# Kernel tuning notes

Hardware: AMD Instinct MI355X
Metric: run time of the kernel (lower is better)

The kernel has to match this reference:

```python
import jax, jax.numpy as jnp
import numpy as np

ALPHA = 3.0   # self.alpha
TAU = 0.1     # contrastive temperature
K = 8         # configs.k (top-k hyperedges per node)


def _scale(x, w, ehy, enod):
    """One scale of incidence_matrix_learn.
    x: [B, L, D] series tokens; w: [ws, D] word tokens;
    ehy: [H, D] hyperedge embedding table; enod: [N, D] node embedding table, N = L + ws.
    Returns (binary incidence matrix [N, H] float32, scalar contrastive loss).
    """
    B = x.shape[0]
    # concat_all[i]: cat(x.permute(0,2,1), word_expanded) -> [B, D, N]
    we = jnp.broadcast_to(w.T[None], (B,) + w.T.shape)          # [B, D, ws]
    concat = jnp.concatenate([jnp.transpose(x, (0, 2, 1)), we], axis=-1)  # [B, D, N]
    N, H = enod.shape[0], ehy.shape[0]
    # adjacency: softmax(relu(alpha * nodeec @ hyperen.T)) along hyperedge dim
    a = enod @ ehy.T                                            # [N, H]
    adj = jax.nn.softmax(jax.nn.relu(ALPHA * a), axis=-1)
    # top-k mask + threshold > 0.5 -> binary incidence matrix
    k = min(H, K)
    _, idx = jax.lax.top_k(adj, k)                              # [N, k]
    mask = jnp.zeros_like(adj).at[jnp.arange(N)[:, None], idx].set(1.0)
    adj_bin = ((adj * mask) > 0.5).astype(jnp.float32)          # [N, H]
    # positives: nodes sharing any hyperedge (build_pos_indices_from_edge_index),
    # equivalent to (A A^T > 0) with self excluded; dropping all-zero columns is a no-op here
    P = (adj_bin @ adj_bin.T > 0) & ~jnp.eye(N, dtype=bool)     # [N, N]
    cnt = P.sum(axis=1)                                         # positives per node
    # acl_loss_batched, vectorized over batch and nodes
    nodes = jnp.transpose(concat, (0, 2, 1))                    # [B, N, D]
    nrm = nodes / jnp.maximum(jnp.linalg.norm(nodes, axis=-1, keepdims=True), 1e-12)
    sim = jnp.einsum('bnd,bmd->bnm', nrm, nrm) / TAU            # [B, N, N]
    denom = jax.nn.logsumexp(sim, axis=-1)                      # [B, N]
    pos_mean = jnp.einsum('bnm,nm->bn', sim, P.astype(sim.dtype)) / jnp.maximum(cnt, 1)
    valid = cnt > 0                                             # [N]
    loss_sum = jnp.sum(jnp.where(valid[None, :], denom - pos_mean, 0.0))
    vc = B * valid.sum()
    loss = jnp.where(vc > 0, loss_sum / jnp.maximum(vc, 1), 0.0)
    return adj_bin, loss


def setup_inputs() -> dict:
    key = jax.random.key(0)
    ks = jax.random.split(key, 8)
    B, D = 64, 512
    return dict(
        x0=jax.random.normal(ks[0], (B, 512, D), dtype=jnp.float32),
        x1=jax.random.normal(ks[1], (B, 256, D), dtype=jnp.float32),
        word0=jax.random.normal(ks[2], (128, D), dtype=jnp.float32),
        word1=jax.random.normal(ks[3], (128, D), dtype=jnp.float32),
        embhy0=jax.random.normal(ks[4], (128, D), dtype=jnp.float32),
        embhy1=jax.random.normal(ks[5], (64, D), dtype=jnp.float32),
        embnod0=jax.random.normal(ks[6], (640, D), dtype=jnp.float32),
        embnod1=jax.random.normal(ks[7], (384, D), dtype=jnp.float32),
    )


def reference(x0, x1, word0, word1, embhy0, embhy1, embnod0, embnod1):
    a0, l0 = _scale(x0, word0, embhy0, embnod0)
    a1, l1 = _scale(x1, word1, embhy1, embnod1)
    return (a0, a1, l0 + l1)
```

## Files before the change

### kernel.cpp

```cpp
#include <hip/hip_runtime.h>


#define DDIM 512
#define BATCH 64

typedef __attribute__((ext_vector_type(8))) short short8;
typedef __attribute__((ext_vector_type(4))) float f32x4;

__device__ __forceinline__ unsigned short f2bf(float f) {
  unsigned int u = __float_as_uint(f);
  u += 0x7fffu + ((u >> 16) & 1u);
  return (unsigned short)(u >> 16);
}

__device__ __forceinline__ void async16(const void* g, void* l) {
  __builtin_amdgcn_global_load_lds(
      (const __attribute__((address_space(1))) unsigned int*)g,
      (__attribute__((address_space(3))) unsigned int*)l, 16, 0, 0);
}

__global__ __launch_bounds__(256) void prep_kernel(
    const float* __restrict__ enod0, const float* __restrict__ ehy0,
    const float* __restrict__ enod1, const float* __restrict__ ehy1,
    float* __restrict__ adj0, float* __restrict__ adj1,
    int* __restrict__ labels0, int* __restrict__ labels1,
    const float* __restrict__ x0, const float* __restrict__ w0,
    const float* __restrict__ x1, const float* __restrict__ w1,
    unsigned short* __restrict__ nhat0, unsigned short* __restrict__ nhat1) {
  const int t = threadIdx.x;
  if (blockIdx.x < 1024) {
    const bool s0 = blockIdx.x < 640;
    const int n = s0 ? blockIdx.x : blockIdx.x - 640;
    const int H = s0 ? 128 : 64;
    const float* enod = s0 ? enod0 : enod1;
    const float* ehy = s0 ? ehy0 : ehy1;
    float* out_adj = s0 ? adj0 : adj1;
    int* labels = s0 ? labels0 : labels1;
    __shared__ float erow[DDIM];
    __shared__ float red[128];
    __shared__ int lab;
    if (t < 128) ((float4*)erow)[t] = ((const float4*)(enod + (size_t)n * DDIM))[t];
    if (t == 0) lab = -1;
    __syncthreads();
    float v = 0.f;
    if (t < H) {
      const float4* hr = (const float4*)(ehy + (size_t)t * DDIM);
      float a = 0.f;
      #pragma unroll 8
      for (int d = 0; d < DDIM / 4; ++d) {
        float4 h = hr[d];
        float4 e = ((const float4*)erow)[d];
        a = fmaf(h.x, e.x, a); a = fmaf(h.y, e.y, a);
        a = fmaf(h.z, e.z, a); a = fmaf(h.w, e.w, a);
      }
      v = fmaxf(0.f, 3.0f * a);
    }
    if (t < 128) red[t] = v;
    __syncthreads();
    for (int s = 64; s > 0; s >>= 1) {
      if (t < s) red[t] = fmaxf(red[t], red[t + s]);
      __syncthreads();
    }
    const float mx = red[0];
    __syncthreads();
    const float e = (t < H) ? __expf(v - mx) : 0.f;
    if (t < 128) red[t] = e;
    __syncthreads();
    for (int s = 64; s > 0; s >>= 1) {
      if (t < s) red[t] += red[t + s];
      __syncthreads();
    }
    const float sum = red[0];
    if (t < H) {
      const float adj = e / sum;
      const float bin = (adj > 0.5f) ? 1.0f : 0.0f;
      out_adj[(size_t)n * H + t] = bin;
      if (bin > 0.f) lab = t;
    }
    __syncthreads();
    if (t == 0) labels[n] = lab;
  } else {
    const int wave = t >> 6;
    const int lane = t & 63;
    const int g = (blockIdx.x - 1024) * 4 + wave;
    const bool s0 = g < BATCH * 640;
    const int gg = s0 ? g : g - BATCH * 640;
    const int N = s0 ? 640 : 384;
    const int L = s0 ? 512 : 256;
    const float* x = s0 ? x0 : x1;
    const float* w = s0 ? w0 : w1;
    unsigned short* nhat = s0 ? nhat0 : nhat1;
    const int b = gg / N;
    const int n = gg - b * N;
    const float* src = (n < L) ? (x + ((size_t)b * L + n) * DDIM)
                               : (w + (size_t)(n - L) * DDIM);
    const float4* rowp = (const float4*)src;
    const float4 v0 = rowp[lane];
    const float4 v1 = rowp[lane + 64];
    float ss = v0.x * v0.x + v0.y * v0.y + v0.z * v0.z + v0.w * v0.w +
               v1.x * v1.x + v1.y * v1.y + v1.z * v1.z + v1.w * v1.w;
    #pragma unroll
    for (int off = 32; off > 0; off >>= 1) ss += __shfl_xor(ss, off);
    const float rinv = 1.0f / fmaxf(sqrtf(ss), 1e-12f);
    ushort4 o0, o1;
    o0.x = f2bf(v0.x * rinv); o0.y = f2bf(v0.y * rinv);
    o0.z = f2bf(v0.z * rinv); o0.w = f2bf(v0.w * rinv);
    o1.x = f2bf(v1.x * rinv); o1.y = f2bf(v1.y * rinv);
    o1.z = f2bf(v1.z * rinv); o1.w = f2bf(v1.w * rinv);
    ushort4* op = (ushort4*)(nhat + ((size_t)b * N + n) * DDIM);
    op[lane] = o0;
    op[lane + 64] = o1;
  }
}

__global__ __launch_bounds__(256) void cnt_kernel(
    const int* __restrict__ labels0, int* __restrict__ cnt0,
    const int* __restrict__ labels1, int* __restrict__ cnt1,
    int* __restrict__ valid) {
  const bool s0 = blockIdx.x == 0;
  const int* labels = s0 ? labels0 : labels1;
  int* cnt = s0 ? cnt0 : cnt1;
  int* validcnt = s0 ? valid : valid + 1;
  const int N = s0 ? 640 : 384;
  __shared__ int lab[640];
  __shared__ int hist[128];
  __shared__ int vc;
  const int t = threadIdx.x;
  if (t == 0) vc = 0;
  if (t < 128) hist[t] = 0;
  for (int i = t; i < N; i += 256) lab[i] = labels[i];
  __syncthreads();
  for (int i = t; i < N; i += 256)
    if (lab[i] >= 0) atomicAdd(&hist[lab[i]], 1);
  __syncthreads();
  int lv = 0;
  for (int i = t; i < N; i += 256) {
    const int c = (lab[i] >= 0) ? hist[lab[i]] - 1 : 0;
    cnt[i] = c;
    if (c > 0) ++lv;
  }
  if (lv > 0) atomicAdd(&vc, lv);
  __syncthreads();
  if (t == 0) *validcnt = vc;
}

__global__ __launch_bounds__(128, 1) void lse_kernel(
    const unsigned short* __restrict__ nhat0, const int* __restrict__ labels0,
    const unsigned short* __restrict__ nhat1, const int* __restrict__ labels1,
    float* __restrict__ seG0, float* __restrict__ posG0,
    float* __restrict__ seG1, float* __restrict__ posG1) {
  __shared__ short8 Bbuf[2][1024];
  __shared__ int labS[640];
  const int tid = threadIdx.x;
  const bool s0 = blockIdx.x < 640;
  const int i = s0 ? blockIdx.x : blockIdx.x - 640;
  const int N = s0 ? 640 : 384;
  const int T = s0 ? 10 : 6;
  const unsigned short* nhat = s0 ? nhat0 : nhat1;
  const int* labels = s0 ? labels0 : labels1;
  float* seG = s0 ? seG0 : seG1;
  float* posG = s0 ? posG0 : posG1;
  const int b = i & 63;
  const int tn = i >> 6;
  const int n0 = tn * 64;
  const int ntj = s0 ? ((tn < 5) ? 6 : 5) : ((tn < 3) ? 4 : 3);
  const int wave = tid >> 6;
  const int lane = tid & 63;
  const int lrow = lane & 15;
  const int lq = lane >> 4;
  for (int t = tid; t < N; t += 128) labS[t] = labels[t];

  const size_t base = (size_t)b * N * DDIM;
  const int rw0 = n0 + wave * 32;
  const unsigned short* Ap0 = nhat + base + (size_t)(rw0 + lrow) * DDIM + lq * 8;
  const unsigned short* Ap1 = nhat + base + (size_t)(rw0 + 16 + lrow) * DDIM + lq * 8;
  short8 a0[16], a1[16];
  #pragma unroll
  for (int ks = 0; ks < 16; ++ks) {
    a0[ks] = *(const short8*)(Ap0 + ks * 32);
    a1[ks] = *(const short8*)(Ap1 + ks * 32);
  }

  const int f0 = wave * 8;
  #pragma unroll
  for (int fi = 0; fi < 8; ++fi) {
    const int f = f0 + fi;
    const int j = f >> 2, ks = f & 3;
    const unsigned short* g = nhat + base +
        (size_t)(n0 + j * 16 + lrow) * DDIM + ks * 32 + lq * 8;
    async16(g, &Bbuf[0][f * 64]);
  }
  __syncthreads();

  int labn[2][4];
  #pragma unroll
  for (int s = 0; s < 2; ++s)
    #pragma unroll
    for (int r = 0; r < 4; ++r) labn[s][r] = labS[rw0 + s * 16 + lq * 4 + r];

  float se[2][4] = {{0.f, 0.f, 0.f, 0.f}, {0.f, 0.f, 0.f, 0.f}};
  float pos[2][4] = {{0.f, 0.f, 0.f, 0.f}, {0.f, 0.f, 0.f, 0.f}};
  const int nchunks = ntj * 4;

  for (int jt = 0; jt < ntj; ++jt) {
    int mt = tn + jt; if (mt >= T) mt -= T;
    const int m0 = mt * 64;
    f32x4 acc[4][2];
    #pragma unroll
    for (int j = 0; j < 4; ++j) {
      acc[j][0] = (f32x4){0.f, 0.f, 0.f, 0.f};
      acc[j][1] = (f32x4){0.f, 0.f, 0.f, 0.f};
    }
    #pragma unroll
    for (int kc = 0; kc < 4; ++kc) {
      const int nc = jt * 4 + kc + 1;
      if (nc < nchunks) {
        const int jt2 = nc >> 2, kc2 = nc & 3;
        int mt2 = tn + jt2; if (mt2 >= T) mt2 -= T;
        short8* dst = &Bbuf[(kc + 1) & 1][0];
        #pragma unroll
        for (int fi = 0; fi < 8; ++fi) {
          const int f = f0 + fi;
          const int j = f >> 2, ks = f & 3;
          const unsigned short* g = nhat + base +
              (size_t)(mt2 * 64 + j * 16 + lrow) * DDIM +
              kc2 * 128 + ks * 32 + lq * 8;
          async16(g, dst + f * 64);
        }
      }
      const short8* bb = &Bbuf[kc & 1][0];
      #pragma unroll
      for (int ks = 0; ks < 4; ++ks) {
        const short8 b0 = bb[(0 + ks) * 64 + lane];
        const short8 b1 = bb[(4 + ks) * 64 + lane];
        const short8 b2 = bb[(8 + ks) * 64 + lane];
        const short8 b3 = bb[(12 + ks) * 64 + lane];
        const short8 av0 = a0[kc * 4 + ks];
        const short8 av1 = a1[kc * 4 + ks];
        acc[0][0] = __builtin_amdgcn_mfma_f32_16x16x32_bf16(av0, b0, acc[0][0], 0, 0, 0);
        acc[0][1] = __builtin_amdgcn_mfma_f32_16x16x32_bf16(av1, b0, acc[0][1], 0, 0, 0);
        acc[1][0] = __builtin_amdgcn_mfma_f32_16x16x32_bf16(av0, b1, acc[1][0], 0, 0, 0);
        acc[1][1] = __builtin_amdgcn_mfma_f32_16x16x32_bf16(av1, b1, acc[1][1], 0, 0, 0);
        acc[2][0] = __builtin_amdgcn_mfma_f32_16x16x32_bf16(av0, b2, acc[2][0], 0, 0, 0);
        acc[2][1] = __builtin_amdgcn_mfma_f32_16x16x32_bf16(av1, b2, acc[2][1], 0, 0, 0);
        acc[3][0] = __builtin_amdgcn_mfma_f32_16x16x32_bf16(av0, b3, acc[3][0], 0, 0, 0);
        acc[3][1] = __builtin_amdgcn_mfma_f32_16x16x32_bf16(av1, b3, acc[3][1], 0, 0, 0);
      }
      __syncthreads();
    }
    float colE[4] = {0.f, 0.f, 0.f, 0.f};
    float colP[4] = {0.f, 0.f, 0.f, 0.f};
    #pragma unroll
    for (int j = 0; j < 4; ++j) {
      const int m = m0 + j * 16 + lrow;
      const int labm = labS[m];
      #pragma unroll
      for (int s = 0; s < 2; ++s) {
        const int row0 = rw0 + s * 16 + lq * 4;
        #pragma unroll
        for (int r = 0; r < 4; ++r) {
          const float sim = acc[j][s][r] * 10.0f;
          const float e = __expf(sim - 10.0f);
          const bool match =
              labn[s][r] >= 0 && labm == labn[s][r] && m != row0 + r;
          const float p = match ? sim : 0.f;
          se[s][r] += e;
          pos[s][r] += p;
          colE[j] += e;
          colP[j] += p;
        }
      }
    }
    if (jt > 0) {
      #pragma unroll
      for (int j = 0; j < 4; ++j) {
        float ce = colE[j], cp = colP[j];
        ce += __shfl_xor(ce, 16); ce += __shfl_xor(ce, 32);
        cp += __shfl_xor(cp, 16); cp += __shfl_xor(cp, 32);
        if (lq == 0) {
          const int m = m0 + j * 16 + lrow;
          atomicAdd(&seG[b * N + m], ce);
          atomicAdd(&posG[b * N + m], cp);
        }
      }
    }
  }

  #pragma unroll
  for (int off = 1; off <= 8; off <<= 1) {
    #pragma unroll
    for (int s = 0; s < 2; ++s)
      #pragma unroll
      for (int r = 0; r < 4; ++r) {
        se[s][r] += __shfl_xor(se[s][r], off);
        pos[s][r] += __shfl_xor(pos[s][r], off);
      }
  }
  if (lrow == 0) {
    #pragma unroll
    for (int s = 0; s < 2; ++s)
      #pragma unroll
      for (int r = 0; r < 4; ++r) {
        const int row = rw0 + s * 16 + lq * 4 + r;
        atomicAdd(&seG[b * N + row], se[s][r]);
        atomicAdd(&posG[b * N + row], pos[s][r]);
      }
  }
}

__global__ __launch_bounds__(256) void reduce_kernel(
    const float* __restrict__ seG0, const float* __restrict__ posG0,
    const int* __restrict__ cnt0, const float* __restrict__ seG1,
    const float* __restrict__ posG1, const int* __restrict__ cnt1,
    float* __restrict__ acc) {
  const int idx = blockIdx.x * 256 + threadIdx.x;
  float v = 0.f;
  int sel;
  if (idx < BATCH * 640) {
    sel = 0;
    const int n = idx % 640;
    const int c = cnt0[n];
    if (c > 0) v = (10.0f + logf(seG0[idx])) - posG0[idx] / (float)c;
  } else {
    sel = 1;
    const int k = idx - BATCH * 640;
    const int n = k % 384;
    const int c = cnt1[n];
    if (c > 0) v = (10.0f + logf(seG1[k])) - posG1[k] / (float)c;
  }
  #pragma unroll
  for (int off = 32; off > 0; off >>= 1) v += __shfl_xor(v, off);
  if ((threadIdx.x & 63) == 0) atomicAdd(&acc[sel], v);
}

__global__ void final_kernel(const float* __restrict__ acc,
                             const int* __restrict__ valid,
                             float* __restrict__ out) {
  float l = 0.f;
  if (valid[0] > 0) l += acc[0] / (float)(BATCH * valid[0]);
  if (valid[1] > 0) l += acc[1] / (float)(BATCH * valid[1]);
  out[0] = l;
}

extern "C" void kernel_launch(void* const* d_in, const int* in_sizes, int n_in,
                              void* d_out, int out_size, void* d_ws,
                              size_t ws_size, hipStream_t stream) {
  const float* x0 = (const float*)d_in[0];
  const float* x1 = (const float*)d_in[1];
  const float* w0 = (const float*)d_in[2];
  const float* w1 = (const float*)d_in[3];
  const float* ehy0 = (const float*)d_in[4];
  const float* ehy1 = (const float*)d_in[5];
  const float* enod0 = (const float*)d_in[6];
  const float* enod1 = (const float*)d_in[7];

  float* out = (float*)d_out;
  float* adj0 = out;
  float* adj1 = out + 640 * 128;
  float* lossp = out + 640 * 128 + 384 * 64;

  unsigned short* nhat0 = (unsigned short*)d_ws;
  unsigned short* nhat1 = nhat0 + (size_t)BATCH * 640 * DDIM;
  int* ip = (int*)(nhat1 + (size_t)BATCH * 384 * DDIM);
  int* labels0 = ip;
  int* labels1 = labels0 + 640;
  int* cnt0 = labels1 + 384;
  int* cnt1 = cnt0 + 640;
  int* valid = cnt1 + 384;
  float* fz = (float*)(valid + 2);
  float* seG0 = fz;
  float* posG0 = seG0 + BATCH * 640;
  float* seG1 = posG0 + BATCH * 640;
  float* posG1 = seG1 + BATCH * 384;
  float* acc = posG1 + BATCH * 384;

  hipMemsetAsync(fz, 0,
                 (size_t)(2 * BATCH * (640 + 384) + 2) * sizeof(float), stream);
  prep_kernel<<<1024 + 16384, 256, 0, stream>>>(
      enod0, ehy0, enod1, ehy1, adj0, adj1, labels0, labels1,
      x0, w0, x1, w1, nhat0, nhat1);
  cnt_kernel<<<2, 256, 0, stream>>>(labels0, cnt0, labels1, cnt1, valid);
  lse_kernel<<<1024, 128, 0, stream>>>(nhat0, labels0, nhat1, labels1,
                                       seG0, posG0, seG1, posG1);
  reduce_kernel<<<256, 256, 0, stream>>>(seG0, posG0, cnt0, seG1, posG1, cnt1,
                                         acc);
  final_kernel<<<1, 1, 0, stream>>>(acc, valid, lossp);
}
```

Measured before the change: 249.5 us.

## Split LSE work into one block per upper-triangular tile pair and fuse small kernels

The similarity kernel now launches one block per (batch, row-tile, column-tile) pair in the upper triangle, 4864 blocks instead of 1024 blocks that each looped over several column tiles. This gives far more parallelism on the many compute units, at the cost of reloading the A fragments for every tile. The memset is folded into extra zeroing blocks of the prep kernel. The count and final kernels are merged into the reduce kernel, which uses a last-block-done counter, cutting launch count.

```diff
diff --git a/kernel.cpp b/kernel.cpp
--- a/kernel.cpp
+++ b/kernel.cpp
@@ -26,7 +26,8 @@
     int* __restrict__ labels0, int* __restrict__ labels1,
     const float* __restrict__ x0, const float* __restrict__ w0,
     const float* __restrict__ x1, const float* __restrict__ w1,
-    unsigned short* __restrict__ nhat0, unsigned short* __restrict__ nhat1) {
+    unsigned short* __restrict__ nhat0, unsigned short* __restrict__ nhat1,
+    float* __restrict__ fz, float* __restrict__ acc, int* __restrict__ done) {
   const int t = threadIdx.x;
   if (blockIdx.x < 1024) {
     const bool s0 = blockIdx.x < 640;
@@ -79,7 +80,7 @@
     }
     __syncthreads();
     if (t == 0) labels[n] = lab;
-  } else {
+  } else if (blockIdx.x < 17408) {
     const int wave = t >> 6;
     const int lane = t & 63;
     const int g = (blockIdx.x - 1024) * 4 + wave;
@@ -110,38 +111,14 @@
     ushort4* op = (ushort4*)(nhat + ((size_t)b * N + n) * DDIM);
     op[lane] = o0;
     op[lane + 64] = o1;
-  }
-}
-
-__global__ __launch_bounds__(256) void cnt_kernel(
-    const int* __restrict__ labels0, int* __restrict__ cnt0,
-    const int* __restrict__ labels1, int* __restrict__ cnt1,
-    int* __restrict__ valid) {
-  const bool s0 = blockIdx.x == 0;
-  const int* labels = s0 ? labels0 : labels1;
-  int* cnt = s0 ? cnt0 : cnt1;
-  int* validcnt = s0 ? valid : valid + 1;
-  const int N = s0 ? 640 : 384;
-  __shared__ int lab[640];
-  __shared__ int hist[128];
-  __shared__ int vc;
-  const int t = threadIdx.x;
-  if (t == 0) vc = 0;
-  if (t < 128) hist[t] = 0;
-  for (int i = t; i < N; i += 256) lab[i] = labels[i];
-  __syncthreads();
-  for (int i = t; i < N; i += 256)
-    if (lab[i] >= 0) atomicAdd(&hist[lab[i]], 1);
-  __syncthreads();
-  int lv = 0;
-  for (int i = t; i < N; i += 256) {
-    const int c = (lab[i] >= 0) ? hist[lab[i]] - 1 : 0;
-    cnt[i] = c;
-    if (c > 0) ++lv;
-  }
-  if (lv > 0) atomicAdd(&vc, lv);
-  __syncthreads();
-  if (t == 0) *validcnt = vc;
+  } else {
+    const int zb = blockIdx.x - 17408;
+    float4* dst = (float4*)fz;
+    const float4 z = {0.f, 0.f, 0.f, 0.f};
+    dst[zb * 512 + t] = z;
+    dst[zb * 512 + t + 256] = z;
+    if (zb == 0 && t == 0) { acc[0] = 0.f; acc[1] = 0.f; *done = 0; }
+  }
 }
 
 __global__ __launch_bounds__(128, 1) void lse_kernel(
@@ -152,18 +129,21 @@
   __shared__ short8 Bbuf[2][1024];
   __shared__ int labS[640];
   const int tid = threadIdx.x;
-  const bool s0 = blockIdx.x < 640;
-  const int i = s0 ? blockIdx.x : blockIdx.x - 640;
+  const bool s0 = blockIdx.x < 3520;
+  const int idx = s0 ? blockIdx.x : blockIdx.x - 3520;
   const int N = s0 ? 640 : 384;
   const int T = s0 ? 10 : 6;
   const unsigned short* nhat = s0 ? nhat0 : nhat1;
   const int* labels = s0 ? labels0 : labels1;
   float* seG = s0 ? seG0 : seG1;
   float* posG = s0 ? posG0 : posG1;
-  const int b = i & 63;
-  const int tn = i >> 6;
-  const int n0 = tn * 64;
-  const int ntj = s0 ? ((tn < 5) ? 6 : 5) : ((tn < 3) ? 4 : 3);
+  const int b = idx & 63;
+  int p = idx >> 6;
+  int i = 0;
+  while (p >= T - i) { p -= T - i; ++i; }
+  const int j = i + p;
+  const int n0 = i * 64;
+  const int m0 = j * 64;
   const int wave = tid >> 6;
   const int lane = tid & 63;
   const int lrow = lane & 15;
@@ -185,9 +165,9 @@
   #pragma unroll
   for (int fi = 0; fi < 8; ++fi) {
     const int f = f0 + fi;
-    const int j = f >> 2, ks = f & 3;
+    const int jf = f >> 2, ks = f & 3;
     const unsigned short* g = nhat + base +
-        (size_t)(n0 + j * 16 + lrow) * DDIM + ks * 32 + lq * 8;
+        (size_t)(m0 + jf * 16 + lrow) * DDIM + ks * 32 + lq * 8;
     async16(g, &Bbuf[0][f * 64]);
   }
   __syncthreads();
@@ -197,95 +177,86 @@
   for (int s = 0; s < 2; ++s)
     #pragma unroll
     for (int r = 0; r < 4; ++r) labn[s][r] = labS[rw0 + s * 16 + lq * 4 + r];
+
+  f32x4 acc[4][2];
+  #pragma unroll
+  for (int jj = 0; jj < 4; ++jj) {
+    acc[jj][0] = (f32x4){0.f, 0.f, 0.f, 0.f};
+    acc[jj][1] = (f32x4){0.f, 0.f, 0.f, 0.f};
+  }
+  #pragma unroll
+  for (int kc = 0; kc < 4; ++kc) {
+    if (kc < 3) {
+      short8* dst = &Bbuf[(kc + 1) & 1][0];
+      #pragma unroll
+      for (int fi = 0; fi < 8; ++fi) {
+        const int f = f0 + fi;
+        const int jf = f >> 2, ks = f & 3;
+        const unsigned short* g = nhat + base +
+            (size_t)(m0 + jf * 16 + lrow) * DDIM +
+            (kc + 1) * 128 + ks * 32 + lq * 8;
+        async16(g, dst + f * 64);
+      }
+    }
+    const short8* bb = &Bbuf[kc & 1][0];
+    #pragma unroll
+    for (int ks = 0; ks < 4; ++ks) {
+      const short8 b0 = bb[(0 + ks) * 64 + lane];
+      const short8 b1 = bb[(4 + ks) * 64 + lane];
+      const short8 b2 = bb[(8 + ks) * 64 + lane];
+      const short8 b3 = bb[(12 + ks) * 64 + lane];
+      const short8 av0 = a0[kc * 4 + ks];
+      const short8 av1 = a1[kc * 4 + ks];
+      acc[0][0] = __builtin_amdgcn_mfma_f32_16x16x32_bf16(av0, b0, acc[0][0], 0, 0, 0);
+      acc[0][1] = __builtin_amdgcn_mfma_f32_16x16x32_bf16(av1, b0, acc[0][1], 0, 0, 0);
+      acc[1][0] = __builtin_amdgcn_mfma_f32_16x16x32_bf16(av0, b1, acc[1][0], 0, 0, 0);
+      acc[1][1] = __builtin_amdgcn_mfma_f32_16x16x32_bf16(av1, b1, acc[1][1], 0, 0, 0);
+      acc[2][0] = __builtin_amdgcn_mfma_f32_16x16x32_bf16(av0, b2, acc[2][0], 0, 0, 0);
+      acc[2][1] = __builtin_amdgcn_mfma_f32_16x16x32_bf16(av1, b2, acc[2][1], 0, 0, 0);
+      acc[3][0] = __builtin_amdgcn_mfma_f32_16x16x32_bf16(av0, b3, acc[3][0], 0, 0, 0);
+      acc[3][1] = __builtin_amdgcn_mfma_f32_16x16x32_bf16(av1, b3, acc[3][1], 0, 0, 0);
+    }
+    if (kc < 3) __syncthreads();
+  }
 
   float se[2][4] = {{0.f, 0.f, 0.f, 0.f}, {0.f, 0.f, 0.f, 0.f}};
   float pos[2][4] = {{0.f, 0.f, 0.f, 0.f}, {0.f, 0.f, 0.f, 0.f}};
-  const int nchunks = ntj * 4;
-
-  for (int jt = 0; jt < ntj; ++jt) {
-    int mt = tn + jt; if (mt >= T) mt -= T;
-    const int m0 = mt * 64;
-    f32x4 acc[4][2];
-    #pragma unroll
-    for (int j = 0; j < 4; ++j) {
-      acc[j][0] = (f32x4){0.f, 0.f, 0.f, 0.f};
-      acc[j][1] = (f32x4){0.f, 0.f, 0.f, 0.f};
-    }
-    #pragma unroll
-    for (int kc = 0; kc < 4; ++kc) {
-      const int nc = jt * 4 + kc + 1;
-      if (nc < nchunks) {
-        const int jt2 = nc >> 2, kc2 = nc & 3;
-        int mt2 = tn + jt2; if (mt2 >= T) mt2 -= T;
-        short8* dst = &Bbuf[(kc + 1) & 1][0];
-        #pragma unroll
-        for (int fi = 0; fi < 8; ++fi) {
-          const int f = f0 + fi;
-          const int j = f >> 2, ks = f & 3;
-          const unsigned short* g = nhat + base +
-              (size_t)(mt2 * 64 + j * 16 + lrow) * DDIM +
-              kc2 * 128 + ks * 32 + lq * 8;
-          async16(g, dst + f * 64);
-        }
-      }
-      const short8* bb = &Bbuf[kc & 1][0];
+  float colE[4] = {0.f, 0.f, 0.f, 0.f};
+  float colP[4] = {0.f, 0.f, 0.f, 0.f};
+  #pragma unroll
+  for (int jj = 0; jj < 4; ++jj) {
+    const int m = m0 + jj * 16 + lrow;
+    const int labm = labS[m];
+    #pragma unroll
+    for (int s = 0; s < 2; ++s) {
+      const int row0 = rw0 + s * 16 + lq * 4;
       #pragma unroll
-      for (int ks = 0; ks < 4; ++ks) {
-        const short8 b0 = bb[(0 + ks) * 64 + lane];
-        const short8 b1 = bb[(4 + ks) * 64 + lane];
-        const short8 b2 = bb[(8 + ks) * 64 + lane];
-        const short8 b3 = bb[(12 + ks) * 64 + lane];
-        const short8 av0 = a0[kc * 4 + ks];
-        const short8 av1 = a1[kc * 4 + ks];
-        acc[0][0] = __builtin_amdgcn_mfma_f32_16x16x32_bf16(av0, b0, acc[0][0], 0, 0, 0);
-        acc[0][1] = __builtin_amdgcn_mfma_f32_16x16x32_bf16(av1, b0, acc[0][1], 0, 0, 0);
-        acc[1][0] = __builtin_amdgcn_mfma_f32_16x16x32_bf16(av0, b1, acc[1][0], 0, 0, 0);
-        acc[1][1] = __builtin_amdgcn_mfma_f32_16x16x32_bf16(av1, b1, acc[1][1], 0, 0, 0);
-        acc[2][0] = __builtin_amdgcn_mfma_f32_16x16x32_bf16(av0, b2, acc[2][0], 0, 0, 0);
-        acc[2][1] = __builtin_amdgcn_mfma_f32_16x16x32_bf16(av1, b2, acc[2][1], 0, 0, 0);
-        acc[3][0] = __builtin_amdgcn_mfma_f32_16x16x32_bf16(av0, b3, acc[3][0], 0, 0, 0);
-        acc[3][1] = __builtin_amdgcn_mfma_f32_16x16x32_bf16(av1, b3, acc[3][1], 0, 0, 0);
-      }
-      __syncthreads();
-    }
-    float colE[4] = {0.f, 0.f, 0.f, 0.f};
-    float colP[4] = {0.f, 0.f, 0.f, 0.f};
-    #pragma unroll
-    for (int j = 0; j < 4; ++j) {
-      const int m = m0 + j * 16 + lrow;
-      const int labm = labS[m];
-      #pragma unroll
-      for (int s = 0; s < 2; ++s) {
-        const int row0 = rw0 + s * 16 + lq * 4;
-        #pragma unroll
-        for (int r = 0; r < 4; ++r) {
-          const float sim = acc[j][s][r] * 10.0f;
-          const float e = __expf(sim - 10.0f);
-          const bool match =
-              labn[s][r] >= 0 && labm == labn[s][r] && m != row0 + r;
-          const float p = match ? sim : 0.f;
-          se[s][r] += e;
-          pos[s][r] += p;
-          colE[j] += e;
-          colP[j] += p;
-        }
-      }
-    }
-    if (jt > 0) {
-      #pragma unroll
-      for (int j = 0; j < 4; ++j) {
-        float ce = colE[j], cp = colP[j];
-        ce += __shfl_xor(ce, 16); ce += __shfl_xor(ce, 32);
-        cp += __shfl_xor(cp, 16); cp += __shfl_xor(cp, 32);
-        if (lq == 0) {
-          const int m = m0 + j * 16 + lrow;
-          atomicAdd(&seG[b * N + m], ce);
-          atomicAdd(&posG[b * N + m], cp);
-        }
-      }
-    }
-  }
-
+      for (int r = 0; r < 4; ++r) {
+        const float sim = acc[jj][s][r] * 10.0f;
+        const float e = __expf(sim - 10.0f);
+        const bool match =
+            labn[s][r] >= 0 && labm == labn[s][r] && m != row0 + r;
+        const float pv = match ? sim : 0.f;
+        se[s][r] += e;
+        pos[s][r] += pv;
+        colE[jj] += e;
+        colP[jj] += pv;
+      }
+    }
+  }
+  if (i != j) {
+    #pragma unroll
+    for (int jj = 0; jj < 4; ++jj) {
+      float ce = colE[jj], cp = colP[jj];
+      ce += __shfl_xor(ce, 16); ce += __shfl_xor(ce, 32);
+      cp += __shfl_xor(cp, 16); cp += __shfl_xor(cp, 32);
+      if (lq == 0) {
+        const int m = m0 + jj * 16 + lrow;
+        atomicAdd(&seG[b * N + m], ce);
+        atomicAdd(&posG[b * N + m], cp);
+      }
+    }
+  }
   #pragma unroll
   for (int off = 1; off <= 8; off <<= 1) {
     #pragma unroll
@@ -310,36 +281,86 @@
 
 __global__ __launch_bounds__(256) void reduce_kernel(
     const float* __restrict__ seG0, const float* __restrict__ posG0,
-    const int* __restrict__ cnt0, const float* __restrict__ seG1,
-    const float* __restrict__ posG1, const int* __restrict__ cnt1,
-    float* __restrict__ acc) {
-  const int idx = blockIdx.x * 256 + threadIdx.x;
+    const float* __restrict__ seG1, const float* __restrict__ posG1,
+    const int* __restrict__ labels0, const int* __restrict__ labels1,
+    float* __restrict__ acc, int* __restrict__ done,
+    float* __restrict__ out_loss) {
+  __shared__ int lab[640];
+  __shared__ int hist[128];
+  __shared__ float bsum[4];
+  __shared__ int flag;
+  const int t = threadIdx.x;
+  const bool s0 = blockIdx.x < 160;
+  const int N = s0 ? 640 : 384;
+  const int H = s0 ? 128 : 64;
+  const int* labels = s0 ? labels0 : labels1;
+  if (t < H) hist[t] = 0;
+  for (int n = t; n < N; n += 256) lab[n] = labels[n];
+  __syncthreads();
+  for (int n = t; n < N; n += 256)
+    if (lab[n] >= 0) atomicAdd(&hist[lab[n]], 1);
+  __syncthreads();
+  const int row = blockIdx.x * 256 + t;
   float v = 0.f;
-  int sel;
-  if (idx < BATCH * 640) {
-    sel = 0;
-    const int n = idx % 640;
-    const int c = cnt0[n];
-    if (c > 0) v = (10.0f + logf(seG0[idx])) - posG0[idx] / (float)c;
+  if (s0) {
+    const int n = row % 640;
+    const int c = (lab[n] >= 0) ? hist[lab[n]] - 1 : 0;
+    if (c > 0) v = (10.0f + logf(seG0[row])) - posG0[row] / (float)c;
   } else {
-    sel = 1;
-    const int k = idx - BATCH * 640;
+    const int k = row - BATCH * 640;
     const int n = k % 384;
-    const int c = cnt1[n];
+    const int c = (lab[n] >= 0) ? hist[lab[n]] - 1 : 0;
     if (c > 0) v = (10.0f + logf(seG1[k])) - posG1[k] / (float)c;
   }
   #pragma unroll
   for (int off = 32; off > 0; off >>= 1) v += __shfl_xor(v, off);
-  if ((threadIdx.x & 63) == 0) atomicAdd(&acc[sel], v);
-}
-
-__global__ void final_kernel(const float* __restrict__ acc,
-                             const int* __restrict__ valid,
-                             float* __restrict__ out) {
-  float l = 0.f;
-  if (valid[0] > 0) l += acc[0] / (float)(BATCH * valid[0]);
-  if (valid[1] > 0) l += acc[1] / (float)(BATCH * valid[1]);
-  out[0] = l;
+  if ((t & 63) == 0) bsum[t >> 6] = v;
+  __syncthreads();
+  if (t == 0) {
+    atomicAdd(&acc[s0 ? 0 : 1], bsum[0] + bsum[1] + bsum[2] + bsum[3]);
+    __threadfence();
+    const int old = atomicAdd(done, 1);
+    flag = (old == (int)gridDim.x - 1) ? 1 : 0;
+  }
+  __syncthreads();
+  if (flag) {
+    __shared__ int h0[128];
+    __shared__ int h1[64];
+    __shared__ int vcnt[2];
+    if (t < 128) h0[t] = 0;
+    if (t < 64) h1[t] = 0;
+    if (t < 2) vcnt[t] = 0;
+    __syncthreads();
+    for (int n = t; n < 640; n += 256) {
+      const int l = labels0[n];
+      if (l >= 0) atomicAdd(&h0[l], 1);
+    }
+    for (int n = t; n < 384; n += 256) {
+      const int l = labels1[n];
+      if (l >= 0) atomicAdd(&h1[l], 1);
+    }
+    __syncthreads();
+    int c0 = 0, c1 = 0;
+    for (int n = t; n < 640; n += 256) {
+      const int l = labels0[n];
+      if (l >= 0 && h0[l] >= 2) ++c0;
+    }
+    for (int n = t; n < 384; n += 256) {
+      const int l = labels1[n];
+      if (l >= 0 && h1[l] >= 2) ++c1;
+    }
+    if (c0 > 0) atomicAdd(&vcnt[0], c0);
+    if (c1 > 0) atomicAdd(&vcnt[1], c1);
+    __syncthreads();
+    if (t == 0) {
+      const float a0 = atomicAdd(&acc[0], 0.0f);
+      const float a1 = atomicAdd(&acc[1], 0.0f);
+      float l = 0.f;
+      if (vcnt[0] > 0) l += a0 / (float)(BATCH * vcnt[0]);
+      if (vcnt[1] > 0) l += a1 / (float)(BATCH * vcnt[1]);
+      *out_loss = l;
+    }
+  }
 }
 
 extern "C" void kernel_launch(void* const* d_in, const int* in_sizes, int n_in,
@@ -361,28 +382,20 @@
 
   unsigned short* nhat0 = (unsigned short*)d_ws;
   unsigned short* nhat1 = nhat0 + (size_t)BATCH * 640 * DDIM;
-  int* ip = (int*)(nhat1 + (size_t)BATCH * 384 * DDIM);
-  int* labels0 = ip;
+  int* labels0 = (int*)(nhat1 + (size_t)BATCH * 384 * DDIM);
   int* labels1 = labels0 + 640;
-  int* cnt0 = labels1 + 384;
-  int* cnt1 = cnt0 + 640;
-  int* valid = cnt1 + 384;
-  float* fz = (float*)(valid + 2);
-  float* seG0 = fz;
+  float* seG0 = (float*)(labels1 + 384);
   float* posG0 = seG0 + BATCH * 640;
   float* seG1 = posG0 + BATCH * 640;
   float* posG1 = seG1 + BATCH * 384;
   float* acc = posG1 + BATCH * 384;
-
-  hipMemsetAsync(fz, 0,
-                 (size_t)(2 * BATCH * (640 + 384) + 2) * sizeof(float), stream);
-  prep_kernel<<<1024 + 16384, 256, 0, stream>>>(
+  int* done = (int*)(acc + 2);
+
+  prep_kernel<<<17472, 256, 0, stream>>>(
       enod0, ehy0, enod1, ehy1, adj0, adj1, labels0, labels1,
-      x0, w0, x1, w1, nhat0, nhat1);
-  cnt_kernel<<<2, 256, 0, stream>>>(labels0, cnt0, labels1, cnt1, valid);
-  lse_kernel<<<1024, 128, 0, stream>>>(nhat0, labels0, nhat1, labels1,
+      x0, w0, x1, w1, nhat0, nhat1, seG0, acc, done);
+  lse_kernel<<<4864, 128, 0, stream>>>(nhat0, labels0, nhat1, labels1,
                                        seG0, posG0, seG1, posG1);
-  reduce_kernel<<<256, 256, 0, stream>>>(seG0, posG0, cnt0, seG1, posG1, cnt1,
-                                         acc);
-  final_kernel<<<1, 1, 0, stream>>>(acc, valid, lossp);
-}
+  reduce_kernel<<<256, 256, 0, stream>>>(seG0, posG0, seG1, posG1,
+                                         labels0, labels1, acc, done, lossp);
+}
```

Result: slower. 261.9 us (+5.0%).
